# Performance work log

Hardware: AMD Instinct MI355X
Metric: run time of the kernel (lower is better)

## Reference

```python
import jax, jax.numpy as jnp
import numpy as np

N = 100000   # nodes
E = 3200000  # edges
F = 128      # num_features
H = 20       # hidden dim (hard-coded in source)
C = 10       # num_classes
EPS = 1e-5


def setup_inputs() -> dict:
    key = jax.random.key(0)
    ks = jax.random.split(key, 16)
    x = jax.random.normal(ks[0], (N, F), jnp.float32)
    edge_index = jax.random.randint(ks[1], (2, E), 0, N)
    edge_weights = jnp.ones((E,), jnp.float32)

    def lin_init(k, fan_in, shape):
        s = 1.0 / np.sqrt(fan_in)
        return jax.random.uniform(k, shape, jnp.float32, -s, s)

    return {
        "x": x,
        "edge_index": edge_index,
        "edge_weights": edge_weights,
        "W1": lin_init(ks[2], F, (F, H)), "b1": jnp.zeros((H,), jnp.float32),
        "g1": jnp.ones((H,), jnp.float32), "be1": jnp.zeros((H,), jnp.float32),
        "W2": lin_init(ks[3], H, (H, H)), "b2": jnp.zeros((H,), jnp.float32),
        "g2": jnp.ones((H,), jnp.float32), "be2": jnp.zeros((H,), jnp.float32),
        "W3": lin_init(ks[4], H, (H, H)), "b3": jnp.zeros((H,), jnp.float32),
        "Wl": lin_init(ks[5], 3 * H, (3 * H, C)), "bl": lin_init(ks[6], 3 * H, (C,)),
    }


def gcn_conv(x, src, dst, ew, W, b, n):
    # PyG GCNConv: transform, add self-loops, symmetric deg^-1/2 normalization, scatter-add.
    h = x @ W  # [N, out]
    loop = jnp.arange(n)
    src2 = jnp.concatenate([src, loop])
    dst2 = jnp.concatenate([dst, loop])
    ew2 = jnp.concatenate([ew, jnp.ones((n,), x.dtype)])
    deg = jax.ops.segment_sum(ew2, dst2, num_segments=n)
    dinv = jnp.where(deg > 0, jax.lax.rsqrt(deg), 0.0)
    coef = (dinv[src2] * ew2 * dinv[dst2])[:, None]  # [E+N, 1]
    out = jax.ops.segment_sum(h[src2] * coef, dst2, num_segments=n)
    return out + b


def batch_norm(x, g, b):
    m = x.mean(axis=0)
    v = x.var(axis=0)
    return (x - m) * jax.lax.rsqrt(v + EPS) * g + b


def reference(x, edge_index, edge_weights, W1, b1, g1, be1, W2, b2, g2, be2, W3, b3, Wl, bl):
    src, dst = edge_index[0], edge_index[1]
    n = x.shape[0]
    o1 = batch_norm(jax.nn.relu(gcn_conv(x, src, dst, edge_weights, W1, b1, n)), g1, be1)
    o2 = batch_norm(jax.nn.relu(gcn_conv(o1, src, dst, edge_weights, W2, b2, n)), g2, be2)
    o3 = jax.nn.relu(gcn_conv(o2, src, dst, edge_weights, W3, b3, n))
    emb = jnp.concatenate([o1, o2, o3], axis=1)  # [N, 60]
    return emb @ Wl + bl
```

## Files before the change

### kernel.cpp

```cpp
#include <hip/hip_runtime.h>
#include <hip/hip_fp16.h>


#define HD 20
#define EPS 1e-5f
#define BSH 7
#define NBMAX 1024
#define CAP 5632
#define CAPE 2816

typedef float __attribute__((ext_vector_type(4))) f4v;

__device__ __forceinline__ float4 ntld4(const float* p) {
    f4v v = __builtin_nontemporal_load((const f4v*)p);
    return make_float4(v.x, v.y, v.z, v.w);
}

__global__ __launch_bounds__(1024)
void init_kernel(int* bcnt, float* stats, float* zero20, int* eflag, int nbv) {
    int t = threadIdx.x;
    if (t < nbv) bcnt[t] = 0;
    if (t < 80) stats[t] = 0.0f;
    if (t < HD) zero20[t] = 0.0f;
    if (t == 0) eflag[0] = 1;
}

__global__ __launch_bounds__(256)
void bucket_hist_kernel(const int* __restrict__ dst, const float* __restrict__ ew,
                        int* __restrict__ bcnt, int* __restrict__ eflag,
                        int E, int chunk, int nbv) {
    __shared__ int lh[NBMAX];
    __shared__ int okf;
    if (threadIdx.x == 0) okf = 1;
    for (int i = threadIdx.x; i < nbv; i += 256) lh[i] = 0;
    __syncthreads();
    int s = blockIdx.x * chunk;
    int e = s + chunk; if (e > E) e = E;
    for (int j = s + threadIdx.x; j < e; j += 256) {
        atomicAdd(&lh[dst[j] >> BSH], 1);
        if (ew[j] != 1.0f) okf = 0;
    }
    __syncthreads();
    for (int i = threadIdx.x; i < nbv; i += 256)
        if (lh[i]) atomicAdd(&bcnt[i], lh[i]);
    if (threadIdx.x == 0 && !okf) eflag[0] = 0;
}

__global__ __launch_bounds__(1024)
void bucket_scan_kernel(const int* __restrict__ bcnt, int* __restrict__ bstart,
                        int* __restrict__ bcur, int* __restrict__ row_start,
                        int n, int E, int nbv) {
    __shared__ int s[1024];
    int t = threadIdx.x;
    int v = (t < nbv) ? bcnt[t] : 0;
    s[t] = v;
    __syncthreads();
    for (int off = 1; off < 1024; off <<= 1) {
        int u = (t >= off) ? s[t - off] : 0;
        __syncthreads();
        s[t] += u;
        __syncthreads();
    }
    if (t < nbv) { int st = s[t] - v; bstart[t] = st; bcur[t] = st; }
    if (t == 0) { bstart[nbv] = E; row_start[n] = E; }
}

__global__ __launch_bounds__(256)
void scatter_kernel(const int* __restrict__ src, const int* __restrict__ dst,
                    const float* __restrict__ ew, const int* __restrict__ eflag,
                    int* __restrict__ bcur, int2* __restrict__ tmp,
                    int E, int chunk, int nbv) {
    __shared__ int lh[NBMAX];
    __shared__ int lbase[NBMAX];
    for (int i = threadIdx.x; i < nbv; i += 256) lh[i] = 0;
    __syncthreads();
    int s = blockIdx.x * chunk;
    int e = s + chunk; if (e > E) e = E;
    for (int j = s + threadIdx.x; j < e; j += 256)
        atomicAdd(&lh[dst[j] >> BSH], 1);
    __syncthreads();
    for (int i = threadIdx.x; i < nbv; i += 256) {
        int c = lh[i];
        lbase[i] = c ? atomicAdd(&bcur[i], c) : 0;
        lh[i] = 0;
    }
    __syncthreads();
    if (eflag[0]) {
        int* tmp4 = (int*)tmp;
        for (int j = s + threadIdx.x; j < e; j += 256) {
            int d = dst[j];
            int b = d >> BSH;
            int pos = atomicAdd(&lh[b], 1);
            tmp4[lbase[b] + pos] = src[j] | ((d & ((1 << BSH) - 1)) << 20);
        }
    } else {
        for (int j = s + threadIdx.x; j < e; j += 256) {
            int d = dst[j];
            int b = d >> BSH;
            int pos = atomicAdd(&lh[b], 1);
            tmp[lbase[b] + pos] = make_int2(src[j] | ((d & ((1 << BSH) - 1)) << 20),
                                           __float_as_int(ew[j]));
        }
    }
}

__global__ __launch_bounds__(256)
void finalize_kernel(const int2* __restrict__ tmp, const int* __restrict__ bstart,
                     const int* __restrict__ eflag,
                     int2* __restrict__ se, int* __restrict__ row_start,
                     float* __restrict__ dinv, int n) {
    __shared__ int hist[128];
    __shared__ float degs[128];
    __shared__ int off[128];
    __shared__ int cur[128];
    __shared__ int2 stage[CAP];
    int* stage4 = (int*)stage;
    const int* tmp4 = (const int*)tmp;
    int* se4 = (int*)se;
    bool f4 = eflag[0] != 0;
    int b = blockIdx.x;
    int s0 = bstart[b], s1 = bstart[b + 1];
    int cnt = s1 - s0;
    int t = threadIdx.x;
    if (t < 128) { hist[t] = 0; degs[t] = 0.0f; cur[t] = 0; }
    __syncthreads();
    if (f4) {
        for (int j = s0 + t; j < s1; j += 256)
            atomicAdd(&hist[tmp4[j] >> 20], 1);
    } else {
        for (int j = s0 + t; j < s1; j += 256) {
            int2 r = tmp[j];
            int l = r.x >> 20;
            atomicAdd(&hist[l], 1);
            atomicAdd(&degs[l], __int_as_float(r.y));
        }
    }
    __syncthreads();
    if (t < 128) off[t] = hist[t];
    __syncthreads();
    for (int o = 1; o < 128; o <<= 1) {
        int u = (t < 128 && t >= o) ? off[t - o] : 0;
        __syncthreads();
        if (t < 128) off[t] += u;
        __syncthreads();
    }
    if (t < 128) {
        int node = (b << BSH) + t;
        if (node < n) {
            row_start[node] = s0 + off[t] - hist[t];
            float dg = f4 ? (float)hist[t] : degs[t];
            dinv[node] = rsqrtf(1.0f + dg);
        }
    }
    __syncthreads();
    if (f4) {
        if (cnt <= 2 * CAP) {
            for (int j = s0 + t; j < s1; j += 256) {
                int r = tmp4[j];
                int l = r >> 20;
                int p = (off[l] - hist[l]) + atomicAdd(&cur[l], 1);
                stage4[p] = r & 0xFFFFF;
            }
            __syncthreads();
            for (int k = t; k < cnt; k += 256) se4[s0 + k] = stage4[k];
        } else {
            for (int j = s0 + t; j < s1; j += 256) {
                int r = tmp4[j];
                int l = r >> 20;
                int p = (off[l] - hist[l]) + atomicAdd(&cur[l], 1);
                se4[s0 + p] = r & 0xFFFFF;
            }
        }
    } else {
        if (cnt <= CAP) {
            for (int j = s0 + t; j < s1; j += 256) {
                int2 r = tmp[j];
                int l = r.x >> 20;
                int p = (off[l] - hist[l]) + atomicAdd(&cur[l], 1);
                stage[p] = make_int2(r.x & 0xFFFFF, r.y);
            }
            __syncthreads();
            for (int k = t; k < cnt; k += 256) se[s0 + k] = stage[k];
        } else {
            for (int j = s0 + t; j < s1; j += 256) {
                int2 r = tmp[j];
                int l = r.x >> 20;
                int p = (off[l] - hist[l]) + atomicAdd(&cur[l], 1);
                se[s0 + p] = make_int2(r.x & 0xFFFFF, r.y);
            }
        }
    }
}

template<int FIN, int NPB>
__global__ __launch_bounds__(256)
void gemm_kernel(const float* __restrict__ in, const float* __restrict__ W,
                 const float* __restrict__ cvec, const float* __restrict__ dinv,
                 __half* __restrict__ hs, int n) {
    __shared__ float sWt[HD][FIN + 4];
    __shared__ float sIn[NPB][FIN + 4];
    __shared__ float sC[HD];
    for (int i = threadIdx.x; i < FIN * HD; i += 256) {
        int k = i / HD, f = i % HD;
        sWt[f][k] = W[i];
    }
    if (threadIdx.x < HD) sC[threadIdx.x] = cvec[threadIdx.x];
    int base = blockIdx.x * NPB;
    int nb = n - base; if (nb > NPB) nb = NPB;
    int lim = n * FIN;
    const int Q = FIN / 4;
    for (int i = threadIdx.x; i < NPB * Q; i += 256) {
        int row = i / Q, c = (i % Q) * 4;
        int g = (base + row) * FIN + c;
        *(float4*)&sIn[row][c] = (g < lim) ? ntld4(&in[g])
                                           : make_float4(0.f, 0.f, 0.f, 0.f);
    }
    __syncthreads();
    for (int idx = threadIdx.x; idx < NPB * 5; idx += 256) {
        int nl = idx / 5, fq = idx % 5;
        float a0 = 0.f, a1 = 0.f, a2 = 0.f, a3 = 0.f;
        #pragma unroll 4
        for (int k = 0; k < FIN; k += 4) {
            float4 x4 = *(const float4*)&sIn[nl][k];
            float4 w0 = *(const float4*)&sWt[4 * fq + 0][k];
            float4 w1 = *(const float4*)&sWt[4 * fq + 1][k];
            float4 w2 = *(const float4*)&sWt[4 * fq + 2][k];
            float4 w3 = *(const float4*)&sWt[4 * fq + 3][k];
            a0 = fmaf(x4.x, w0.x, a0); a0 = fmaf(x4.y, w0.y, a0);
            a0 = fmaf(x4.z, w0.z, a0); a0 = fmaf(x4.w, w0.w, a0);
            a1 = fmaf(x4.x, w1.x, a1); a1 = fmaf(x4.y, w1.y, a1);
            a1 = fmaf(x4.z, w1.z, a1); a1 = fmaf(x4.w, w1.w, a1);
            a2 = fmaf(x4.x, w2.x, a2); a2 = fmaf(x4.y, w2.y, a2);
            a2 = fmaf(x4.z, w2.z, a2); a2 = fmaf(x4.w, w2.w, a2);
            a3 = fmaf(x4.x, w3.x, a3); a3 = fmaf(x4.y, w3.y, a3);
            a3 = fmaf(x4.z, w3.z, a3); a3 = fmaf(x4.w, w3.w, a3);
        }
        if (nl < nb) {
            int node = base + nl;
            float di = dinv[node];
            __half2 h01 = __floats2half2_rn((a0 + sC[4 * fq + 0]) * di,
                                            (a1 + sC[4 * fq + 1]) * di);
            __half2 h23 = __floats2half2_rn((a2 + sC[4 * fq + 2]) * di,
                                            (a3 + sC[4 * fq + 3]) * di);
            uint2 pk = make_uint2(*(unsigned*)&h01, *(unsigned*)&h23);
            *(uint2*)&hs[(size_t)node * HD + 4 * fq] = pk;
        }
    }
}

#define FMA4(A, V, W) \
    A.x = fmaf(V.x, W, A.x); A.y = fmaf(V.y, W, A.y); \
    A.z = fmaf(V.z, W, A.z); A.w = fmaf(V.w, W, A.w);

#define ADD4(A, V) \
    A.x += V.x; A.y += V.y; A.z += V.z; A.w += V.w;

__device__ __forceinline__ float4 h4f2(uint2 u) {
    float2 f0 = __half22float2(*reinterpret_cast<const __half2*>(&u.x));
    float2 f1 = __half22float2(*reinterpret_cast<const __half2*>(&u.y));
    return make_float4(f0.x, f0.y, f1.x, f1.y);
}

#define ROWLD(Q0, Q1, Q2, SRC) { \
    const char* rp_ = (const char*)hsb + (size_t)(SRC) * 40; \
    Q0 = *(const uint4*)rp_; \
    Q1 = *(const uint4*)(rp_ + 16); \
    Q2 = *(const uint2*)(rp_ + 32); }

#define AGG_LOOP(EDGEAT)                                                     \
    {                                                                        \
        int2 e = EDGEAT(j);                                                  \
        float w = __int_as_float(e.y);                                       \
        uint4 c0, c1; uint2 c2; ROWLD(c0, c1, c2, e.x)                       \
        while (true) {                                                       \
            int jn = j + 4;                                                  \
            bool more = jn < s1;                                             \
            int jp = more ? jn : j;                                          \
            int2 en = EDGEAT(jp);                                            \
            uint4 n0, n1; uint2 n2; ROWLD(n0, n1, n2, en.x)                  \
            float wn = __int_as_float(en.y);                                 \
            float4 v0 = h4f2(make_uint2(c0.x, c0.y));                        \
            float4 v1 = h4f2(make_uint2(c0.z, c0.w));                        \
            float4 v2 = h4f2(make_uint2(c1.x, c1.y));                        \
            float4 v3 = h4f2(make_uint2(c1.z, c1.w));                        \
            float4 v4 = h4f2(c2);                                            \
            FMA4(a0, v0, w) FMA4(a1, v1, w) FMA4(a2, v2, w)                  \
            FMA4(a3, v3, w) FMA4(a4, v4, w)                                  \
            if (!more) break;                                                \
            j = jn; w = wn;                                                  \
            c0 = n0; c1 = n1; c2 = n2;                                       \
        }                                                                    \
    }

#define AGG_LOOP4(EDGEAT)                                                    \
    {                                                                        \
        int e = EDGEAT(j);                                                   \
        uint4 c0, c1; uint2 c2; ROWLD(c0, c1, c2, e)                         \
        while (true) {                                                       \
            int jn = j + 4;                                                  \
            bool more = jn < s1;                                             \
            int jp = more ? jn : j;                                          \
            int en = EDGEAT(jp);                                             \
            uint4 n0, n1; uint2 n2; ROWLD(n0, n1, n2, en)                    \
            float4 v0 = h4f2(make_uint2(c0.x, c0.y));                        \
            float4 v1 = h4f2(make_uint2(c0.z, c0.w));                        \
            float4 v2 = h4f2(make_uint2(c1.x, c1.y));                        \
            float4 v3 = h4f2(make_uint2(c1.z, c1.w));                        \
            float4 v4 = h4f2(c2);                                            \
            ADD4(a0, v0) ADD4(a1, v1) ADD4(a2, v2)                           \
            ADD4(a3, v3) ADD4(a4, v4)                                        \
            if (!more) break;                                                \
            j = jn;                                                          \
            c0 = n0; c1 = n1; c2 = n2;                                       \
        }                                                                    \
    }

#define EDGE_LDS(jj)  sse[(jj) - sb0]
#define EDGE_GBL(jj)  se[(jj)]
#define EDGE_LDS4(jj) sse4[(jj) - sb0]
#define EDGE_GBL4(jj) se4[(jj)]

template<int MODE>
__global__ __launch_bounds__(256)
void agg_kernel(const __half* __restrict__ hsb, const float* __restrict__ dinv,
                const int* __restrict__ row_start, const int2* __restrict__ se,
                const int* __restrict__ eflag,
                const float* __restrict__ bias, float* __restrict__ out,
                float* __restrict__ stat_sum, float* __restrict__ stat_sq,
                const float* __restrict__ o1, const float* __restrict__ o2,
                const float* __restrict__ Wlp, const float* __restrict__ blp,
                int n) {
    __shared__ int2 sse[CAPE];
    int* sse4 = (int*)sse;
    const int* se4 = (const int*)se;
    __shared__ float ls[HD], lq[HD];
    __shared__ float sW[600];
    __shared__ float sb[10];
    bool f4 = eflag[0] != 0;
    int base = blockIdx.x * 64;
    int nEnd = base + 64; if (nEnd > n) nEnd = n;
    int sb0 = row_start[base];
    int sb1 = row_start[nEnd];
    int span = sb1 - sb0;
    bool ok = span <= (f4 ? 2 * CAPE : CAPE);
    if (MODE == 0) {
        if (threadIdx.x < HD) { ls[threadIdx.x] = 0.0f; lq[threadIdx.x] = 0.0f; }
    } else {
        for (int i = threadIdx.x; i < 600; i += 256) sW[i] = Wlp[i];
        if (threadIdx.x < 10) sb[threadIdx.x] = blp[threadIdx.x];
    }
    if (ok) {
        if (f4) {
            for (int k = threadIdx.x; k < span; k += 256)
                sse4[k] = __builtin_nontemporal_load(se4 + sb0 + k);
        } else {
            for (int k = threadIdx.x; k < span; k += 256) {
                long long v = __builtin_nontemporal_load(
                    (const long long*)(se + sb0 + k));
                sse[k] = *(const int2*)&v;
            }
        }
    }
    __syncthreads();
    int i = base + (threadIdx.x >> 2), lane = threadIdx.x & 3;
    if (i < n) {
        float di = dinv[i];
        int s0 = row_start[i], s1 = row_start[i + 1];
        float4 a0, a1, a2, a3, a4;
        if (lane == 0) {
            uint4 y0, y1; uint2 y2;
            ROWLD(y0, y1, y2, i)
            a0 = h4f2(make_uint2(y0.x, y0.y));
            a1 = h4f2(make_uint2(y0.z, y0.w));
            a2 = h4f2(make_uint2(y1.x, y1.y));
            a3 = h4f2(make_uint2(y1.z, y1.w));
            a4 = h4f2(y2);
        } else {
            a0 = a1 = a2 = a3 = a4 = make_float4(0.f, 0.f, 0.f, 0.f);
        }
        int j = s0 + lane;
        if (j < s1) {
            if (f4) {
                if (ok) { AGG_LOOP4(EDGE_LDS4) }
                else    { AGG_LOOP4(EDGE_GBL4) }
            } else {
                if (ok) { AGG_LOOP(EDGE_LDS) }
                else    { AGG_LOOP(EDGE_GBL) }
            }
        }
        #define REDX(A, M) \
            A.x += __shfl_xor(A.x, M); A.y += __shfl_xor(A.y, M); \
            A.z += __shfl_xor(A.z, M); A.w += __shfl_xor(A.w, M);
        #define RED4L(A) REDX(A, 1) REDX(A, 2)
        RED4L(a0) RED4L(a1) RED4L(a2) RED4L(a3) RED4L(a4)
        float4 acc[5] = {a0, a1, a2, a3, a4};
        float va[HD];
        #pragma unroll
        for (int q = 0; q < 5; ++q) {
            float4 bb = *(const float4*)(bias + 4 * q);
            va[4 * q + 0] = fmaxf(fmaf(acc[q].x, di, bb.x), 0.0f);
            va[4 * q + 1] = fmaxf(fmaf(acc[q].y, di, bb.y), 0.0f);
            va[4 * q + 2] = fmaxf(fmaf(acc[q].z, di, bb.z), 0.0f);
            va[4 * q + 3] = fmaxf(fmaf(acc[q].w, di, bb.w), 0.0f);
        }
        if (MODE == 0) {
            if (lane == 0) {
                #pragma unroll
                for (int q = 0; q < 5; ++q) {
                    ((float4*)out)[i * 5 + q] = make_float4(
                        va[4 * q], va[4 * q + 1], va[4 * q + 2], va[4 * q + 3]);
                    int f = 4 * q;
                    atomicAdd(&ls[f + 0], va[f + 0]); atomicAdd(&lq[f + 0], va[f + 0] * va[f + 0]);
                    atomicAdd(&ls[f + 1], va[f + 1]); atomicAdd(&lq[f + 1], va[f + 1] * va[f + 1]);
                    atomicAdd(&ls[f + 2], va[f + 2]); atomicAdd(&lq[f + 2], va[f + 2] * va[f + 2]);
                    atomicAdd(&ls[f + 3], va[f + 3]); atomicAdd(&lq[f + 3], va[f + 3] * va[f + 3]);
                }
            }
        } else {
            float r1[HD], r2[HD];
            #pragma unroll
            for (int q = 0; q < 5; ++q) {
                *(float4*)&r1[4 * q] = ((const float4*)(o1 + (size_t)i * HD))[q];
                *(float4*)&r2[4 * q] = ((const float4*)(o2 + (size_t)i * HD))[q];
            }
            for (int c = lane; c < 10; c += 4) {
                float s = sb[c];
                #pragma unroll
                for (int k = 0; k < HD; ++k) s = fmaf(r1[k], sW[k * 10 + c], s);
                #pragma unroll
                for (int k = 0; k < HD; ++k) s = fmaf(r2[k], sW[(HD + k) * 10 + c], s);
                #pragma unroll
                for (int k = 0; k < HD; ++k) s = fmaf(va[k], sW[(2 * HD + k) * 10 + c], s);
                out[(size_t)i * 10 + c] = s;
            }
        }
    }
    if (MODE == 0) {
        __syncthreads();
        if (threadIdx.x < HD) {
            atomicAdd(&stat_sum[threadIdx.x], ls[threadIdx.x]);
            atomicAdd(&stat_sq[threadIdx.x], lq[threadIdx.x]);
        }
    }
}

__global__ __launch_bounds__(512)
void bn_adjust_kernel(const float* __restrict__ sum, const float* __restrict__ sq,
                      const float* __restrict__ g, const float* __restrict__ be,
                      const float* __restrict__ W, float* __restrict__ scsh_out,
                      float* __restrict__ Wp, float* __restrict__ cvec, int n) {
    __shared__ float ssc[HD], ssh[HD];
    int t = threadIdx.x;
    if (t < HD) {
        float inv_n = 1.0f / (float)n;
        float m = sum[t] * inv_n;
        float var = sq[t] * inv_n - m * m;
        float sc = g[t] * rsqrtf(var + EPS);
        float sh = be[t] - m * sc;
        ssc[t] = sc; ssh[t] = sh;
        scsh_out[t] = sc; scsh_out[HD + t] = sh;
    }
    __syncthreads();
    if (t < HD * HD) Wp[t] = ssc[t / HD] * W[t];
    if (t < HD) {
        float acc = 0.0f;
        #pragma unroll
        for (int k = 0; k < HD; ++k) acc = fmaf(ssh[k], W[k * HD + t], acc);
        cvec[t] = acc;
    }
}

__global__ __launch_bounds__(640)
void bn_adjust2_kernel(const float* __restrict__ sum, const float* __restrict__ sq,
                       const float* __restrict__ g, const float* __restrict__ be,
                       const float* __restrict__ W, float* __restrict__ scsh_out,
                       float* __restrict__ Wp, float* __restrict__ cvec,
                       const float* __restrict__ Wl, const float* __restrict__ bl,
                       const float* __restrict__ scsh1,
                       float* __restrict__ Wlp, float* __restrict__ blp, int n) {
    __shared__ float ssc[HD], ssh[HD];
    int t = threadIdx.x;
    if (t < HD) {
        float inv_n = 1.0f / (float)n;
        float m = sum[t] * inv_n;
        float var = sq[t] * inv_n - m * m;
        float sc = g[t] * rsqrtf(var + EPS);
        float sh = be[t] - m * sc;
        ssc[t] = sc; ssh[t] = sh;
        scsh_out[t] = sc; scsh_out[HD + t] = sh;
    }
    __syncthreads();
    if (t < HD * HD) Wp[t] = ssc[t / HD] * W[t];
    if (t < HD) {
        float acc = 0.0f;
        #pragma unroll
        for (int k = 0; k < HD; ++k) acc = fmaf(ssh[k], W[k * HD + t], acc);
        cvec[t] = acc;
    }
    if (t < 600) {
        int k = t / 10;
        float s = (k < HD) ? scsh1[k] : (k < 2 * HD) ? ssc[k - HD] : 1.0f;
        Wlp[t] = s * Wl[t];
    }
    if (t < 10) {
        float acc = bl[t];
        #pragma unroll
        for (int k = 0; k < HD; ++k) acc = fmaf(scsh1[HD + k], Wl[k * 10 + t], acc);
        #pragma unroll
        for (int k = 0; k < HD; ++k) acc = fmaf(ssh[k], Wl[(HD + k) * 10 + t], acc);
        blp[t] = acc;
    }
}

extern "C" void kernel_launch(void* const* d_in, const int* in_sizes, int n_in,
                              void* d_out, int out_size, void* d_ws, size_t ws_size,
                              hipStream_t stream) {
    const float* x   = (const float*)d_in[0];
    const int*   ei  = (const int*)d_in[1];
    const float* ew  = (const float*)d_in[2];
    const float* W1  = (const float*)d_in[3];
    const float* b1  = (const float*)d_in[4];
    const float* g1  = (const float*)d_in[5];
    const float* be1 = (const float*)d_in[6];
    const float* W2  = (const float*)d_in[7];
    const float* b2  = (const float*)d_in[8];
    const float* g2  = (const float*)d_in[9];
    const float* be2 = (const float*)d_in[10];
    const float* W3  = (const float*)d_in[11];
    const float* b3  = (const float*)d_in[12];
    const float* Wl  = (const float*)d_in[13];
    const float* bl  = (const float*)d_in[14];
    float* out = (float*)d_out;

    const int F = in_sizes[3] / HD;
    const int N = in_sizes[0] / F;
    const int E = in_sizes[2];
    const int* src = ei;
    const int* dst = ei + E;
    const int nbv = (N + 127) >> BSH;

    char* p = (char*)d_ws;
    auto alloc = [&](size_t bytes) -> void* {
        void* r = (void*)p;
        p += (bytes + 255) & ~(size_t)255;
        return r;
    };
    size_t nh4 = (size_t)N * HD * 4;
    int2*  se      = (int2*) alloc((size_t)E * 8);
    char*  regionA = (char*) alloc((size_t)E * 8);
    float* o2r     = (float*)alloc(nh4);
    float* dinv    = (float*)alloc((size_t)N * 4);
    int*   row_start = (int*)alloc((size_t)(N + 1) * 4);
    int*   bcnt    = (int*)  alloc(NBMAX * 4);
    int*   bstart  = (int*)  alloc((NBMAX + 1) * 4);
    int*   bcur    = (int*)  alloc(NBMAX * 4);
    float* stats   = (float*)alloc(80 * 4);
    float* scsh    = (float*)alloc(80 * 4);
    float* zero20  = (float*)alloc(20 * 4);
    float* W2p     = (float*)alloc(400 * 4);
    float* c2      = (float*)alloc(20 * 4);
    float* W3p     = (float*)alloc(400 * 4);
    float* c3      = (float*)alloc(20 * 4);
    float* Wlp     = (float*)alloc(600 * 4);
    float* blp     = (float*)alloc(12 * 4);
    int*   eflag   = (int*)  alloc(4);

    int2*   tmp = (int2*)regionA;
    __half* hs  = (__half*)regionA;
    float*  o1r = (float*)(regionA + 2 * nh4);

    const int B = 256;
    const int GB = 1024;
    const int chunk = (E + GB - 1) / GB;
    int gAgg = (4 * N + B - 1) / B;

    hipLaunchKernelGGL(init_kernel, dim3(1), dim3(1024), 0, stream,
                       bcnt, stats, zero20, eflag, nbv);
    hipLaunchKernelGGL(bucket_hist_kernel, dim3(GB), dim3(B), 0, stream,
                       dst, ew, bcnt, eflag, E, chunk, nbv);
    hipLaunchKernelGGL(bucket_scan_kernel, dim3(1), dim3(1024), 0, stream,
                       bcnt, bstart, bcur, row_start, N, E, nbv);
    hipLaunchKernelGGL(scatter_kernel, dim3(GB), dim3(B), 0, stream,
                       src, dst, ew, eflag, bcur, tmp, E, chunk, nbv);
    hipLaunchKernelGGL(finalize_kernel, dim3(nbv), dim3(B), 0, stream,
                       tmp, bstart, eflag, se, row_start, dinv, N);

    hipLaunchKernelGGL((gemm_kernel<128, 16>), dim3((N + 15) / 16), dim3(B), 0, stream,
                       x, W1, zero20, dinv, hs, N);
    hipLaunchKernelGGL((agg_kernel<0>), dim3(gAgg), dim3(B), 0, stream,
                       hs, dinv, row_start, se, eflag, b1, o1r,
                       stats, stats + 20, nullptr, nullptr, nullptr, nullptr, N);
    hipLaunchKernelGGL(bn_adjust_kernel, dim3(1), dim3(512), 0, stream,
                       stats, stats + 20, g1, be1, W2, scsh, W2p, c2, N);

    hipLaunchKernelGGL((gemm_kernel<HD, 64>), dim3((N + 63) / 64), dim3(B), 0, stream,
                       o1r, W2p, c2, dinv, hs, N);
    hipLaunchKernelGGL((agg_kernel<0>), dim3(gAgg), dim3(B), 0, stream,
                       hs, dinv, row_start, se, eflag, b2, o2r,
                       stats + 40, stats + 60, nullptr, nullptr, nullptr, nullptr, N);
    hipLaunchKernelGGL(bn_adjust2_kernel, dim3(1), dim3(640), 0, stream,
                       stats + 40, stats + 60, g2, be2, W3, scsh + 40, W3p, c3,
                       Wl, bl, scsh, Wlp, blp, N);

    hipLaunchKernelGGL((gemm_kernel<HD, 64>), dim3((N + 63) / 64), dim3(B), 0, stream,
                       o2r, W3p, c3, dinv, hs, N);
    hipLaunchKernelGGL((agg_kernel<1>), dim3(gAgg), dim3(B), 0, stream,
                       hs, dinv, row_start, se, eflag, b3, out,
                       nullptr, nullptr, o1r, o2r, Wlp, blp, N);
}
```

Before: 523.9 us.

## Stage bucket scatter in shared memory for contiguous global writes

In the scatter kernel's unit-weight path, each block now computes a local exclusive scan of its bucket histogram, sorts its chunk of edges by bucket into shared memory, then writes them out linearly so consecutive threads store to consecutive addresses within each bucket's global region. This is meant to replace scattered 4-byte global stores with mostly coalesced runs. The grid is halved to 512 blocks so each chunk (6250 edges) fits the 6400-entry staging buffer. The cost is a block-wide scan with extra barriers, a large shared-memory footprint that lowers occupancy, and fewer blocks in flight for the histogram and scatter phases.

```diff
diff --git a/kernel.cpp b/kernel.cpp
--- a/kernel.cpp
+++ b/kernel.cpp
@@ -8,6 +8,7 @@
 #define NBMAX 1024
 #define CAP 5632
 #define CAPE 2816
+#define CHUNKMAX 6400
 
 typedef float __attribute__((ext_vector_type(4))) f4v;
 
@@ -71,35 +72,83 @@
                     int* __restrict__ bcur, int2* __restrict__ tmp,
                     int E, int chunk, int nbv) {
     __shared__ int lh[NBMAX];
+    __shared__ int lofs[NBMAX];
     __shared__ int lbase[NBMAX];
-    for (int i = threadIdx.x; i < nbv; i += 256) lh[i] = 0;
-    __syncthreads();
+    __shared__ int sc[256];
+    __shared__ int stage[CHUNKMAX];
+    __shared__ unsigned short sbid[CHUNKMAX];
+    int t = threadIdx.x;
     int s = blockIdx.x * chunk;
     int e = s + chunk; if (e > E) e = E;
-    for (int j = s + threadIdx.x; j < e; j += 256)
+    int cnt = e - s;
+    bool f4 = eflag[0] != 0;
+    for (int i = t; i < nbv; i += 256) lh[i] = 0;
+    __syncthreads();
+    for (int j = s + t; j < e; j += 256)
         atomicAdd(&lh[dst[j] >> BSH], 1);
     __syncthreads();
-    for (int i = threadIdx.x; i < nbv; i += 256) {
-        int c = lh[i];
-        lbase[i] = c ? atomicAdd(&bcur[i], c) : 0;
-        lh[i] = 0;
-    }
-    __syncthreads();
-    if (eflag[0]) {
-        int* tmp4 = (int*)tmp;
-        for (int j = s + threadIdx.x; j < e; j += 256) {
+    if (f4 && cnt <= CHUNKMAX) {
+        int base4 = t * 4;
+        int v0 = 0, v1 = 0, v2 = 0, v3 = 0, tsum = 0;
+        if (base4 + 0 < nbv) { v0 = lh[base4 + 0]; tsum += v0; }
+        if (base4 + 1 < nbv) { v1 = lh[base4 + 1]; tsum += v1; }
+        if (base4 + 2 < nbv) { v2 = lh[base4 + 2]; tsum += v2; }
+        if (base4 + 3 < nbv) { v3 = lh[base4 + 3]; tsum += v3; }
+        sc[t] = tsum;
+        __syncthreads();
+        for (int off = 1; off < 256; off <<= 1) {
+            int u = (t >= off) ? sc[t - off] : 0;
+            __syncthreads();
+            sc[t] += u;
+            __syncthreads();
+        }
+        int ex = sc[t] - tsum;
+        if (base4 + 0 < nbv) { lofs[base4 + 0] = ex; ex += v0; }
+        if (base4 + 1 < nbv) { lofs[base4 + 1] = ex; ex += v1; }
+        if (base4 + 2 < nbv) { lofs[base4 + 2] = ex; ex += v2; }
+        if (base4 + 3 < nbv) { lofs[base4 + 3] = ex; ex += v3; }
+        for (int i = t; i < nbv; i += 256) {
+            int c = lh[i];
+            lbase[i] = c ? atomicAdd(&bcur[i], c) : 0;
+            lh[i] = 0;
+        }
+        __syncthreads();
+        for (int j = s + t; j < e; j += 256) {
             int d = dst[j];
             int b = d >> BSH;
-            int pos = atomicAdd(&lh[b], 1);
-            tmp4[lbase[b] + pos] = src[j] | ((d & ((1 << BSH) - 1)) << 20);
+            int p = lofs[b] + atomicAdd(&lh[b], 1);
+            stage[p] = src[j] | ((d & ((1 << BSH) - 1)) << 20);
+            sbid[p] = (unsigned short)b;
+        }
+        __syncthreads();
+        int* tmp4 = (int*)tmp;
+        for (int k = t; k < cnt; k += 256) {
+            int b = sbid[k];
+            tmp4[lbase[b] + (k - lofs[b])] = stage[k];
         }
     } else {
-        for (int j = s + threadIdx.x; j < e; j += 256) {
-            int d = dst[j];
-            int b = d >> BSH;
-            int pos = atomicAdd(&lh[b], 1);
-            tmp[lbase[b] + pos] = make_int2(src[j] | ((d & ((1 << BSH) - 1)) << 20),
-                                           __float_as_int(ew[j]));
+        for (int i = t; i < nbv; i += 256) {
+            int c = lh[i];
+            lbase[i] = c ? atomicAdd(&bcur[i], c) : 0;
+            lh[i] = 0;
+        }
+        __syncthreads();
+        if (f4) {
+            int* tmp4 = (int*)tmp;
+            for (int j = s + t; j < e; j += 256) {
+                int d = dst[j];
+                int b = d >> BSH;
+                int pos = atomicAdd(&lh[b], 1);
+                tmp4[lbase[b] + pos] = src[j] | ((d & ((1 << BSH) - 1)) << 20);
+            }
+        } else {
+            for (int j = s + t; j < e; j += 256) {
+                int d = dst[j];
+                int b = d >> BSH;
+                int pos = atomicAdd(&lh[b], 1);
+                tmp[lbase[b] + pos] = make_int2(src[j] | ((d & ((1 << BSH) - 1)) << 20),
+                                               __float_as_int(ew[j]));
+            }
         }
     }
 }
@@ -570,7 +619,7 @@
     float*  o1r = (float*)(regionA + 2 * nh4);
 
     const int B = 256;
-    const int GB = 1024;
+    const int GB = 512;
     const int chunk = (E + GB - 1) / GB;
     int gAgg = (4 * N + B - 1) / B;
 
```

Measured after the change: 489.3 us. 1.07x faster.
